# Performance work log

Measured on AMD Instinct MI355X. Metric: run time of the kernel, lower is better.

## Reference

```python
import jax, jax.numpy as jnp
import numpy as np

EPS = 1e-9
WINDOW = 5
TEMP = 1.0


def _ln(x, g, b):
    m = jnp.mean(x, -1, keepdims=True)
    v = jnp.mean((x - m) ** 2, -1, keepdims=True)
    return (x - m) * jax.lax.rsqrt(v + 1e-5) * g + b


def setup_inputs() -> dict:
    key = jax.random.key(0)
    ks = jax.random.split(key, 20)
    N, S, D, H, W = 32, 512, 256, 1024, WINDOW
    sd = 0.02
    inp = {
        'sequence': jax.random.normal(ks[0], (N, S, D), jnp.float32),
        'input_mask': jnp.ones((N, S, 1), jnp.float32),
        'START': jax.random.normal(ks[1], (D,), jnp.float32),
        'END': jax.random.normal(ks[2], (D,), jnp.float32),
        'yes_t': jax.random.normal(ks[3], (1, 1, D), jnp.float32),
        'no_t': jax.random.normal(ks[4], (1, 1, D), jnp.float32),
        'convW': jax.random.normal(ks[5], (W * D, D), jnp.float32) * sd,
        'convb': jnp.zeros((D,), jnp.float32),
        'scW': jax.random.normal(ks[6], (D, 1), jnp.float32) * sd,
        'scb': jnp.zeros((1,), jnp.float32),
        'itW': jax.random.normal(ks[7], (D, D), jnp.float32) * sd,
        'itb': jnp.zeros((D,), jnp.float32),
        'w1W': jax.random.normal(ks[8], (2 * D, H), jnp.float32) * sd,
        'w1b': jnp.zeros((H,), jnp.float32),
        'w2W': jax.random.normal(ks[9], (H, 4 * D), jnp.float32) * sd,
        'w2b': jnp.zeros((4 * D,), jnp.float32),
        'lng': jnp.ones((D,), jnp.float32),
        'lnb': jnp.zeros((D,), jnp.float32),
        'n_steps': 6,
    }
    return inp


def _forward(sequence, input_mask, START, END, yes_t, no_t, convW, convb, scW, scb,
             itW, itb, w1W, w1b, w2W, w2b, lng, lnb, n_steps):
    N, S, D = sequence.shape
    dt = sequence.dtype
    # ---- augment_sequence: add soft START / END tokens ----
    seq = jnp.concatenate([jnp.broadcast_to(START.reshape(1, 1, D), (N, 1, D)), sequence], 1)
    mask = jnp.concatenate([jnp.ones((N, 1, 1), dt), input_mask], 1)            # (N,S+1,1)
    mask_no_end = jnp.concatenate([mask, jnp.zeros((N, 1, 1), dt)], 1)          # (N,S+2,1)
    mask_yes_end = jnp.concatenate([jnp.ones((N, 1, 1), dt), mask], 1)
    END_mask = mask_yes_end - mask_no_end
    seq = jnp.concatenate([seq, jnp.zeros((N, 1, D), dt)], 1)                   # (N,S+2,D)
    seq = END_mask * END.reshape(1, 1, D) + (1 - END_mask) * seq
    mask = mask_yes_end
    mask_no_start = jnp.concatenate([jnp.zeros((N, 1, 1), dt), mask[:, 1:]], 1)
    S2 = S + 2
    last_token_mask = jnp.concatenate([END_mask[:, 1:], jnp.zeros((N, 1, 1), dt)], 1)
    selp = mask_no_start * mask_no_end * (1.0 - last_token_mask)                # START_END_LAST_PAD_mask

    active = jnp.ones((N, S2, 1), dt) * mask
    ltp = jnp.zeros((N, S2, 1), dt)
    seq = _ln(seq @ itW + itb, lng, lnb) * mask                                 # initial_transform

    def neighbor_probs(active, mask):
        am = jnp.swapaxes(mask, 1, 2)                                           # (N,1,S2)
        ap = jnp.swapaxes(active, 1, 2)
        am2 = jnp.stack([am[:, :, ::-1], am], 1)                                # (N,2,1,S2)
        ap2 = jnp.stack([ap[:, :, ::-1], ap], 1)
        mat = jnp.broadcast_to(ap2, (N, 2, S2, S2)) * am2                       # (N,2,S2,S2)
        right_exist = jnp.triu(mat, 1)
        log_not = jnp.triu(jnp.log(1.0 - right_exist + EPS), 1)
        not_yet = jnp.exp(jnp.cumsum(log_not, -1))
        not_yet = jnp.concatenate([jnp.ones((N, 2, S2, 1), dt), not_yet[..., :-1]], -1)
        rp = right_exist * not_yet * am2
        left = rp[:, 0][:, ::-1, ::-1]                                          # flip dims (1,2)
        right = rp[:, 1]
        return left, right

    for _ in range(n_steps):
        lnp, rnp = neighbor_probs(active, mask)
        tf = ltp * yes_t + (1 - ltp) * no_t
        base = seq + tf
        lk, rk = base, base
        lefts, rights = [], []
        for _k in range(WINDOW // 2):                                           # k-hop soft neighbors
            lk = lnp @ lk
            lefts = [lk] + lefts
            rk = rnp @ rk
            rights = rights + [rk]
        ws = jnp.stack(lefts + [base] + rights, -2)                             # (N,S2,W,D)
        flat = ws.reshape(N, S2, WINDOW * D)
        tsc = (jax.nn.gelu(flat @ convW + convb) @ scW + scb)[..., 0:1] / TEMP
        mx = jnp.maximum(jnp.max(tsc), 0.0)                                     # no-op score is 0
        et = jnp.exp(tsc - mx) * selp
        en = jnp.exp(-mx)
        tp = et / (et + en + EPS)                                               # transition prob
        # ---- composer (gated cell) on (left child, self) ----
        left_child = lnp @ seq
        cc = jnp.concatenate([left_child, seq], -1)
        inter = jax.nn.gelu(cc @ w1W + w1b)
        contents = (inter @ w2W + w2b).reshape(N, S2, 4, D)
        gates = jax.nn.sigmoid(contents[:, :, :3])
        parent = contents[:, :, 3]
        comp = _ln(gates[:, :, 0] * left_child + gates[:, :, 1] * seq + gates[:, :, 2] * parent, lng, lnb)
        seq = (tp * comp + (1 - tp) * seq) * mask
        # left child of a transitioning node becomes inactive
        deact = jnp.einsum('bij,bi->bj', lnp, tp[..., 0])[..., None]
        active = jnp.clip(active * (1.0 - deact), 0.0, 1.0) * mask
        ltp = tp
    return seq


def reference(sequence, input_mask, START, END, yes_t, no_t, convW, convb, scW, scb,
              itW, itb, w1W, w1b, w2W, w2b, lng, lnb, n_steps):
    return _forward(sequence, input_mask, START, END, yes_t, no_t, convW, convb, scW, scb,
                    itW, itb, w1W, w1b, w2W, w2b, lng, lnb, int(n_steps))
```

## Files before the change

kernel.cpp:

```cpp
#include <hip/hip_runtime.h>
#include <math.h>

#define NB 32
#define SS 512
#define S2 514
#define DD 256
#define HH 1024
#define MS (NB*S2)
#define MP 16512
#define EPSF 1e-9f
#define NSTEPS 6
#define NCH 9

typedef unsigned short ushort_t;
typedef __attribute__((ext_vector_type(8))) short short8;
typedef __attribute__((ext_vector_type(4))) float f32x4;

__device__ __forceinline__ float gelu_f(float x){
  float t = tanhf(0.7978845608028654f*(x + 0.044715f*x*x*x));
  return 0.5f*x*(1.f+t);
}
__device__ __forceinline__ float sigmoid_f(float x){ return 1.f/(1.f+expf(-x)); }
__device__ __forceinline__ ushort_t f2bf(float f){
  unsigned u = __float_as_uint(f);
  u += 0x7fffu + ((u>>16)&1u);
  return (ushort_t)(u>>16);
}
__device__ __forceinline__ float bf2f(ushort_t b){
  return __uint_as_float(((unsigned)b)<<16);
}
__device__ __forceinline__ void gload_lds16(const void* g, void* l){
  __builtin_amdgcn_global_load_lds((const __attribute__((address_space(1))) void*)g,
                                   (__attribute__((address_space(3))) void*)l, 16, 0, 0);
}

__global__ __launch_bounds__(256) void k_wt(const float* __restrict__ W, ushort_t* __restrict__ WT,
                                            int K, int N){
  __shared__ float t[64][65];
  int k0 = blockIdx.x*64, n0 = blockIdx.y*64;
  int tx = threadIdx.x & 63, ty = threadIdx.x >> 6;
#pragma unroll
  for (int i=ty;i<64;i+=4) t[i][tx] = W[(size_t)(k0+i)*N + n0 + tx];
  __syncthreads();
#pragma unroll
  for (int i=ty;i<64;i+=4) WT[(size_t)(n0+i)*K + k0 + tx] = f2bf(t[tx][i]);
}

__global__ void k_build_seq0(const float* __restrict__ seq_in, const float* __restrict__ START,
                             const float* __restrict__ END, ushort_t* __restrict__ out){
  int m = blockIdx.x; int d = threadIdx.x;
  int s = m % S2; int b = m / S2;
  float v;
  if (s == 0)        v = START[d];
  else if (s <= SS)  v = seq_in[((size_t)(b*SS + (s-1)))*DD + d];
  else               v = END[d];
  out[(size_t)m*DD + d] = f2bf(v);
}

__global__ void k_init_state(float* __restrict__ ltp, float* __restrict__ act){
  int i = blockIdx.x*256 + threadIdx.x;
  if (i < MS){ ltp[i]=0.f; act[i]=1.f; }
}

template<int ACT, int OUTBF, int SCORE>
__global__ __launch_bounds__(256) void k_mgemm(const ushort_t* __restrict__ A,
    const ushort_t* __restrict__ BT, const float* __restrict__ bias,
    float* __restrict__ Cf, ushort_t* __restrict__ Cb,
    const float* __restrict__ scW, float* __restrict__ tsc,
    int M, int N, int K)
{
  __shared__ __align__(16) ushort_t Asm[2][128*32];
  __shared__ __align__(16) ushort_t Bsm[2][128*32];
  const int tid = threadIdx.x;
  const int lane = tid & 63, wid = tid >> 6;

  const int nwg = gridDim.x, f = blockIdx.x;
  const int q = nwg >> 3, r = nwg & 7;
  const int x = f & 7, jj = f >> 3;
  const int logical = (x < r ? x*(q+1) : r*(q+1) + (x-r)*q) + jj;
  const int NX = N >> 7;
  const int bx = logical % NX, by = logical / NX;
  const int m0 = by * 128, n0 = bx * 128;
  const int wr = (wid>>1)*64, wc = (wid&1)*64;

  f32x4 acc[4][4];
#pragma unroll
  for (int i=0;i<4;i++)
#pragma unroll
    for (int j=0;j<4;j++) acc[i][j] = (f32x4){0.f,0.f,0.f,0.f};

  const int srow4 = lane >> 2;
  const int scol = ((((lane&3) - (lane>>3)) & 3) << 3);
  const int rrow = lane & 15, rhi = lane >> 4;

  const int nt = K >> 5;
  int cur = 0;

#pragma unroll
  for (int tt=0; tt<2; ++tt){
    int c = wid + 4*tt;
    gload_lds16(A  + (size_t)(m0 + c*16 + srow4)*K + scol, &Asm[0][c*512]);
    gload_lds16(BT + (size_t)(n0 + c*16 + srow4)*K + scol, &Bsm[0][c*512]);
  }
  asm volatile("s_waitcnt vmcnt(0)\n\ts_barrier" ::: "memory");

  for (int t=0; t<nt; ++t){
    if (t+1 < nt){
      const int k1 = (t+1) << 5;
#pragma unroll
      for (int tt=0; tt<2; ++tt){
        int c = wid + 4*tt;
        gload_lds16(A  + (size_t)(m0 + c*16 + srow4)*K + k1 + scol, &Asm[cur^1][c*512]);
        gload_lds16(BT + (size_t)(n0 + c*16 + srow4)*K + k1 + scol, &Bsm[cur^1][c*512]);
      }
    }
    short8 a[4], b[4];
#pragma unroll
    for (int i=0;i<4;i++){
      int ra = wr + i*16 + rrow;
      int sa = ((rhi + (ra>>1)) & 3) << 3;
      a[i] = *reinterpret_cast<const short8*>(&Asm[cur][ra*32 + sa]);
      int rb = wc + i*16 + rrow;
      int sb = ((rhi + (rb>>1)) & 3) << 3;
      b[i] = *reinterpret_cast<const short8*>(&Bsm[cur][rb*32 + sb]);
    }
    __builtin_amdgcn_s_setprio(1);
#pragma unroll
    for (int i=0;i<4;i++)
#pragma unroll
      for (int j=0;j<4;j++)
        acc[i][j] = __builtin_amdgcn_mfma_f32_16x16x32_bf16(a[i], b[j], acc[i][j], 0,0,0);
    __builtin_amdgcn_s_setprio(0);
    if (t+1 < nt){
      asm volatile("s_waitcnt vmcnt(0)\n\ts_barrier" ::: "memory");
      cur ^= 1;
    }
  }

  if (SCORE){
#pragma unroll
    for (int i=0;i<4;i++){
#pragma unroll
      for (int rreg=0;rreg<4;rreg++){
        float rs = 0.f;
#pragma unroll
        for (int j=0;j<4;j++){
          int gn = n0 + wc + j*16 + (lane&15);
          float v = gelu_f(acc[i][j][rreg] + bias[gn]);
          rs += v * scW[gn];
        }
        rs += __shfl_xor(rs,1); rs += __shfl_xor(rs,2);
        rs += __shfl_xor(rs,4); rs += __shfl_xor(rs,8);
        if ((lane&15)==0){
          int gm = m0 + wr + i*16 + (lane>>4)*4 + rreg;
          atomicAdd(&tsc[gm], rs);
        }
      }
    }
  } else {
#pragma unroll
    for (int i=0;i<4;i++){
#pragma unroll
      for (int rreg=0;rreg<4;rreg++){
        size_t gm = m0 + wr + i*16 + (lane>>4)*4 + rreg;
#pragma unroll
        for (int j=0;j<4;j++){
          int gn = n0 + wc + j*16 + (lane&15);
          float v = acc[i][j][rreg] + bias[gn];
          if (ACT==1) v = gelu_f(v);
          if (OUTBF) Cb[gm*N + gn] = f2bf(v);
          else       Cf[gm*N + gn] = v;
        }
      }
    }
  }
}

__global__ __launch_bounds__(256) void k_ln(const float* __restrict__ x, const float* __restrict__ g,
                                            const float* __restrict__ bta, float* __restrict__ out,
                                            ushort_t* __restrict__ cc){
  __shared__ float red[8];
  int m = blockIdx.x, d = threadIdx.x;
  float v = x[(size_t)m*DD + d];
  float s1 = v, s2 = v*v;
  for (int off=32; off; off>>=1){ s1 += __shfl_down(s1,off); s2 += __shfl_down(s2,off); }
  int wid = d >> 6;
  if ((d&63)==0){ red[wid*2]=s1; red[wid*2+1]=s2; }
  __syncthreads();
  float sum = red[0]+red[2]+red[4]+red[6];
  float sq  = red[1]+red[3]+red[5]+red[7];
  float mean = sum * (1.f/DD);
  float var  = sq  * (1.f/DD) - mean*mean;
  float inv  = rsqrtf(fmaxf(var,0.f) + 1e-5f);
  float o = (v-mean)*inv*g[d] + bta[d];
  out[(size_t)m*DD + d] = o;
  cc[(size_t)m*(2*DD) + DD + d] = f2bf(o);
}

template<int PASS>
__global__ __launch_bounds__(64) void k_scanchunk(
    const ushort_t* __restrict__ ccp, const float* __restrict__ ltpp, const float* __restrict__ actp,
    const float* __restrict__ yes_t, const float* __restrict__ no_t,
    ushort_t* __restrict__ ws5, ushort_t* __restrict__ ccw,
    float* __restrict__ carry, float* __restrict__ scal)
{
  __shared__ ushort_t s_sv[66][64];
  __shared__ float s_lt[66], s_ac[66];
  const int b = blockIdx.x, dg = blockIdx.y & 3, ck = blockIdx.y >> 2, dir = blockIdx.z, t = threadIdx.x;
  int st, ln;
  if (dir==0){ st = ck*64; ln = (S2 - st < 64) ? (S2 - st) : 64; }
  else { int hi = (S2-1) - ck*64; st = (hi-63 < 0) ? 0 : hi-63; ln = hi - st + 1; }
  const int lo = st - 1;
  const size_t mb = (size_t)b*S2;
  for (int r=0; r<ln+2; ++r){
    int gr = lo + r; gr = gr < 0 ? 0 : (gr > S2-1 ? S2-1 : gr);
    s_sv[r][t] = ccp[(mb+gr)*(2*DD) + DD + (dg<<6) + t];
  }
  for (int r=t; r<ln+2; r+=64){
    int gr = lo + r; gr = gr < 0 ? 0 : (gr > S2-1 ? S2-1 : gr);
    s_lt[r] = ltpp[mb+gr]; s_ac[r] = actp[mb+gr];
  }
  __syncthreads();
  const int d = (dg<<6)+t;
  const float yv = yes_t[d], nv = no_t[d];
  float ci1=0.f, ci2=0.f, cic=0.f;
  const size_t cbase = (((size_t)b*2+dir)*NCH + ck)*3*DD;
  if (PASS==1){
    ci1 = carry[cbase+d]; ci2 = carry[cbase+DD+d];
    if (dir==0) cic = carry[cbase+2*DD+d];
  }
  float A=1.f, Bs=0.f, z1=0.f, z2=0.f, zc=0.f;
  const int pr = (dir==0) ? 0 : (ln+1);
  float svp = bf2f(s_sv[pr][t]); float ltpv = s_lt[pr];
  float pb = svp + ltpv*yv + (1.f-ltpv)*nv, ps = svp, pa = s_ac[pr];
  for (int i=0;i<ln;i++){
    const int r = (dir==0) ? (i+1) : (ln-i);
    const int s = (dir==0) ? (st+i) : (st+ln-1-i);
    float sv = bf2f(s_sv[r][t]); float lt = s_lt[r]; float av = s_ac[r];
    float bse = sv + lt*yv + (1.f-lt)*nv;
    bool upd = (dir==0) ? (s>0) : (s<S2-1);
    if (upd){
      float c = pa, fc = 1.f-c+EPSF;
      z2 = c*z1 + fc*z2;
      z1 = c*pb + fc*z1;
      zc = c*ps + fc*zc;
      Bs = c*A + fc*Bs; A = fc*A;
    }
    if (PASS==1){
      size_t m = mb + s; size_t w5 = m*(5*DD);
      float Z1 = z1 + A*ci1, Z2 = z2 + Bs*ci1 + A*ci2;
      if (dir==0){
        float Zc = zc + A*cic;
        ws5[w5 + d]        = f2bf(Z2);
        ws5[w5 + DD + d]   = f2bf(Z1);
        ws5[w5 + 2*DD + d] = f2bf(bse);
        ccw[m*(2*DD) + d]  = f2bf(Zc);
      } else {
        ws5[w5 + 3*DD + d] = f2bf(Z1);
        ws5[w5 + 4*DD + d] = f2bf(Z2);
      }
    }
    pb=bse; ps=sv; pa=av;
  }
  if (PASS==0){
    carry[cbase+d] = z1; carry[cbase+DD+d] = z2;
    if (dir==0) carry[cbase+2*DD+d] = zc;
    if (dg==0 && t==0){ size_t sb = (((size_t)b*2+dir)*NCH+ck)*2; scal[sb]=A; scal[sb+1]=Bs; }
  }
}

__global__ __launch_bounds__(64) void k_scancomb(const float* __restrict__ cl, float* __restrict__ cin,
    const float* __restrict__ scal, float* __restrict__ tscp, const float* __restrict__ scb,
    unsigned* __restrict__ mxp)
{
  const int b = blockIdx.x, dg = blockIdx.y, dir = blockIdx.z, t = threadIdx.x;
  const int d = (dg<<6)+t;
  if (dir==0 && dg==0){
    float sbv = scb[0];
    for (int i=t;i<S2;i+=64) tscp[(size_t)b*S2+i]=sbv;
    if (b==0 && t==0) *mxp = 0u;
  }
  float s1=0.f,s2=0.f,sc=0.f;
  for (int k=0;k<NCH;k++){
    size_t cbase = (((size_t)b*2+dir)*NCH+k)*3*DD;
    cin[cbase+d]=s1; cin[cbase+DD+d]=s2; if(dir==0) cin[cbase+2*DD+d]=sc;
    size_t sb = (((size_t)b*2+dir)*NCH+k)*2;
    float A = scal[sb], Bs = scal[sb+1];
    float l1 = cl[cbase+d], l2 = cl[cbase+DD+d];
    float ns1 = l1 + A*s1;
    float ns2 = l2 + Bs*s1 + A*s2;
    if (dir==0){ float lcv = cl[cbase+2*DD+d]; sc = lcv + A*sc; }
    s1=ns1; s2=ns2;
  }
}

__global__ __launch_bounds__(256) void k_maxred(const float* __restrict__ tsc, unsigned* __restrict__ mx){
  __shared__ float red[4];
  int t0 = blockIdx.x*256 + threadIdx.x;
  float v = 0.f;
  for (int i=t0; i<MS; i+=256*32) v = fmaxf(v, tsc[i]);
  for (int off=32; off; off>>=1) v = fmaxf(v, __shfl_down(v,off));
  if ((threadIdx.x&63)==0) red[threadIdx.x>>6]=v;
  __syncthreads();
  if (threadIdx.x==0){
    float r = fmaxf(fmaxf(red[0],red[1]),fmaxf(red[2],red[3]));
    atomicMax(mx, __float_as_uint(r));
  }
}

__global__ __launch_bounds__(256) void k_epi(const ushort_t* __restrict__ contents,
     const float* __restrict__ tsc, const unsigned* __restrict__ mx,
     const float* __restrict__ g, const float* __restrict__ bta,
     float* __restrict__ seq, ushort_t* __restrict__ cc, float* __restrict__ ltp){
  __shared__ float red[8];
  int m = blockIdx.x, d = threadIdx.x;
  int s = m % S2;
  float M = __uint_as_float(*mx);
  float sel = (s >= 1 && s <= SS-1) ? 1.f : 0.f;
  float et = expf(tsc[m]-M)*sel;
  float tpv = et/(et+expf(-M)+EPSF);
  if (d==0) ltp[m] = tpv;

  size_t b4 = (size_t)m*HH;
  float lcv = bf2f(cc[(size_t)m*(2*DD) + d]);
  float sv  = seq[(size_t)m*DD+d];
  float g0 = sigmoid_f(bf2f(contents[b4 + d]));
  float g1 = sigmoid_f(bf2f(contents[b4 + DD + d]));
  float g2 = sigmoid_f(bf2f(contents[b4 + 2*DD + d]));
  float pv = bf2f(contents[b4 + 3*DD + d]);
  float xv = g0*lcv + g1*sv + g2*pv;
  float s1=xv, s2=xv*xv;
  for (int off=32; off; off>>=1){ s1 += __shfl_down(s1,off); s2 += __shfl_down(s2,off); }
  int wid = d>>6;
  if ((d&63)==0){ red[wid*2]=s1; red[wid*2+1]=s2; }
  __syncthreads();
  float sum=red[0]+red[2]+red[4]+red[6];
  float sq =red[1]+red[3]+red[5]+red[7];
  float mean = sum*(1.f/DD);
  float var  = sq *(1.f/DD)-mean*mean;
  float inv = rsqrtf(fmaxf(var,0.f)+1e-5f);
  float comp = (xv-mean)*inv*g[d] + bta[d];
  float o = tpv*comp + (1.f-tpv)*sv;
  seq[(size_t)m*DD+d] = o;
  cc[(size_t)m*(2*DD) + DD + d] = f2bf(o);
}

__global__ __launch_bounds__(64) void k_actup(const float* __restrict__ tp, float* __restrict__ act){
  __shared__ float s_a[S2], s_t[S2], s_o[S2];
  int b = blockIdx.x, t = threadIdx.x;
  for (int s=t;s<S2;s+=64){ s_a[s]=act[(size_t)b*S2+s]; s_t[s]=tp[(size_t)b*S2+s]; }
  __syncthreads();
  int hi = (S2-1) - 9*t;
  int lo = hi - 8; if (lo < 0) lo = 0;
  float A=1.f, Bv=0.f;
  if (hi >= 0){
    for (int s=hi; s>=lo; --s){
      float fc = 1.f - s_a[s] + EPSF;
      Bv = s_t[s] + fc*Bv; A = fc*A;
    }
  }
  float Ai=A, Bi=Bv;
  for (int off=1; off<64; off<<=1){
    float Ao = __shfl_up(Ai, off), Bo = __shfl_up(Bi, off);
    if (t >= off){ Bi = Bi + Ai*Bo; Ai = Ai*Ao; }
  }
  float uin = __shfl_up(Bi, 1); if (t==0) uin = 0.f;
  if (hi >= 0){
    float u = uin;
    for (int s=hi; s>=lo; --s){
      float a = s_a[s];
      float na = a*(1.f - a*u);
      s_o[s] = fminf(fmaxf(na,0.f),1.f);
      u = s_t[s] + (1.f - a + EPSF)*u;
    }
  }
  __syncthreads();
  for (int s=t;s<S2;s+=64) act[(size_t)b*S2+s]=s_o[s];
}

extern "C" void kernel_launch(void* const* d_in, const int* in_sizes, int n_in,
                              void* d_out, int out_size, void* d_ws, size_t ws_size,
                              hipStream_t stream){
  const float* seq_in = (const float*)d_in[0];
  const float* START = (const float*)d_in[2];
  const float* END   = (const float*)d_in[3];
  const float* yes_t = (const float*)d_in[4];
  const float* no_t  = (const float*)d_in[5];
  const float* convW = (const float*)d_in[6];
  const float* convb = (const float*)d_in[7];
  const float* scW   = (const float*)d_in[8];
  const float* scb   = (const float*)d_in[9];
  const float* itW   = (const float*)d_in[10];
  const float* itb   = (const float*)d_in[11];
  const float* w1W   = (const float*)d_in[12];
  const float* w1b   = (const float*)d_in[13];
  const float* w2W   = (const float*)d_in[14];
  const float* w2b   = (const float*)d_in[15];
  const float* lng   = (const float*)d_in[16];
  const float* lnb   = (const float*)d_in[17];

  char* p = (char*)d_ws;
  float*    seq  = (float*)p;    p += (size_t)MP*DD*4;
  ushort_t* cc   = (ushort_t*)p; p += (size_t)MP*(2*DD)*2;
  ushort_t* ws5      = (ushort_t*)p;
  ushort_t* contents = (ushort_t*)p;
  float*    preLN    = (float*)p; p += (size_t)MP*2560;
  ushort_t* inter = (ushort_t*)p;
  ushort_t* seq0  = (ushort_t*)p; p += (size_t)MP*2048;
  ushort_t* itWT   = (ushort_t*)p; p += (size_t)256*256*2;
  ushort_t* convWT = (ushort_t*)p; p += (size_t)256*1280*2;
  ushort_t* w1WT   = (ushort_t*)p; p += (size_t)1024*512*2;
  ushort_t* w2WT   = (ushort_t*)p; p += (size_t)1024*1024*2;
  float* ltp = (float*)p; p += (size_t)MS*4;
  float* act = (float*)p; p += (size_t)MS*4;
  float* tsc = (float*)p; p += (size_t)MP*4;
  unsigned* mx = (unsigned*)p; p += 256;
  float* carryL = (float*)p; p += (size_t)NB*2*NCH*3*DD*4;
  float* carryI = (float*)p; p += (size_t)NB*2*NCH*3*DD*4;
  float* scal   = (float*)p; p += (size_t)NB*2*NCH*2*4;

  dim3 b256(256), b64(64);

  { dim3 g(256/64, 256/64);   k_wt<<<g, b256, 0, stream>>>(itW,  itWT,  256, 256); }
  { dim3 g(1280/64, 256/64);  k_wt<<<g, b256, 0, stream>>>(convW,convWT,1280,256); }
  { dim3 g(512/64, 1024/64);  k_wt<<<g, b256, 0, stream>>>(w1W,  w1WT,  512, 1024); }
  { dim3 g(1024/64, 1024/64); k_wt<<<g, b256, 0, stream>>>(w2W,  w2WT,  1024,1024); }

  k_build_seq0<<<MS, 256, 0, stream>>>(seq_in, START, END, seq0);
  { int nwg = (256/128)*(MP/128);
    k_mgemm<0,0,0><<<nwg, b256, 0, stream>>>(seq0, itWT, itb, preLN, nullptr, nullptr, nullptr, MP, 256, 256); }
  k_ln<<<MS, 256, 0, stream>>>(preLN, lng, lnb, seq, cc);
  k_init_state<<<(MS+255)/256, 256, 0, stream>>>(ltp, act);

  for (int step=0; step<NSTEPS; ++step){
    { dim3 g(NB, 4*NCH, 2);
      k_scanchunk<0><<<g, b64, 0, stream>>>(cc, ltp, act, yes_t, no_t, ws5, cc, carryL, scal); }
    { dim3 g(NB, 4, 2);
      k_scancomb<<<g, b64, 0, stream>>>(carryL, carryI, scal, tsc, scb, mx); }
    { dim3 g(NB, 4*NCH, 2);
      k_scanchunk<1><<<g, b64, 0, stream>>>(cc, ltp, act, yes_t, no_t, ws5, cc, carryI, scal); }
    { int nwg = (256/128)*(MP/128);
      k_mgemm<0,0,1><<<nwg, b256, 0, stream>>>(ws5, convWT, convb, nullptr, nullptr, scW, tsc, MP, 256, 5*DD); }
    k_maxred<<<32, b256, 0, stream>>>(tsc, mx);
    { int nwg = (HH/128)*(MP/128);
      k_mgemm<1,1,0><<<nwg, b256, 0, stream>>>(cc, w1WT, w1b, nullptr, inter, nullptr, nullptr, MP, HH, 2*DD); }
    { int nwg = (HH/128)*(MP/128);
      k_mgemm<0,1,0><<<nwg, b256, 0, stream>>>(inter, w2WT, w2b, nullptr, contents, nullptr, nullptr, MP, HH, HH); }
    k_epi<<<MS, 256, 0, stream>>>(contents, tsc, mx, lng, lnb, seq, cc, ltp);
    k_actup<<<NB, b64, 0, stream>>>(ltp, act);
  }
  hipMemcpyAsync(d_out, seq, (size_t)out_size*sizeof(float), hipMemcpyDeviceToDevice, stream);
}
```

Measured before the change: 1.376 ms.

## Fuse scan combine and max-reduction into neighbours; use 128x64 tiles for N=256 GEMMs

Removes the separate scan-combine kernel by having each pass-1 chunk recompute its carry-in from the preceding chunk summaries, and moves tsc/mx initialisation into pass-0. The global max-reduction over scores is folded into the first 32 blocks of the w1 GEMM, and the N=256 GEMMs switch to 128x64 tiles to launch more workgroups. This cuts two launches per step and improves occupancy for narrow GEMMs, at the cost of redundant carry recomputation and extra work in some GEMM blocks.

```diff
diff --git a/kernel.cpp b/kernel.cpp
--- a/kernel.cpp
+++ b/kernel.cpp
@@ -62,30 +62,47 @@
   if (i < MS){ ltp[i]=0.f; act[i]=1.f; }
 }
 
-template<int ACT, int OUTBF, int SCORE>
+template<int ACT, int OUTBF, int SCORE, int NTILE, int DOMAX>
 __global__ __launch_bounds__(256) void k_mgemm(const ushort_t* __restrict__ A,
     const ushort_t* __restrict__ BT, const float* __restrict__ bias,
     float* __restrict__ Cf, ushort_t* __restrict__ Cb,
-    const float* __restrict__ scW, float* __restrict__ tsc,
+    const float* __restrict__ scW, float* __restrict__ tsc, unsigned* __restrict__ mxp,
     int M, int N, int K)
 {
   __shared__ __align__(16) ushort_t Asm[2][128*32];
-  __shared__ __align__(16) ushort_t Bsm[2][128*32];
+  __shared__ __align__(16) ushort_t Bsm[2][NTILE*32];
   const int tid = threadIdx.x;
   const int lane = tid & 63, wid = tid >> 6;
+
+  if (DOMAX){
+    if (blockIdx.x < 32){
+      __shared__ float redm[4];
+      float v = 0.f;
+      for (int i = blockIdx.x*256 + tid; i < MS; i += 8192) v = fmaxf(v, tsc[i]);
+      for (int off=32; off; off>>=1) v = fmaxf(v, __shfl_down(v,off));
+      if ((tid&63)==0) redm[tid>>6]=v;
+      __syncthreads();
+      if (tid==0){
+        float r = fmaxf(fmaxf(redm[0],redm[1]),fmaxf(redm[2],redm[3]));
+        atomicMax(mxp, __float_as_uint(r));
+      }
+    }
+  }
 
   const int nwg = gridDim.x, f = blockIdx.x;
   const int q = nwg >> 3, r = nwg & 7;
   const int x = f & 7, jj = f >> 3;
   const int logical = (x < r ? x*(q+1) : r*(q+1) + (x-r)*q) + jj;
-  const int NX = N >> 7;
+  const int NX = N / NTILE;
   const int bx = logical % NX, by = logical / NX;
-  const int m0 = by * 128, n0 = bx * 128;
-  const int wr = (wid>>1)*64, wc = (wid&1)*64;
+  const int m0 = by * 128, n0 = bx * NTILE;
+  const int MI = (NTILE==128) ? 4 : 2;
+  const int wr = (NTILE==128) ? (wid>>1)*64 : wid*32;
+  const int wc = (NTILE==128) ? (wid&1)*64  : 0;
 
   f32x4 acc[4][4];
 #pragma unroll
-  for (int i=0;i<4;i++)
+  for (int i=0;i<MI;i++)
 #pragma unroll
     for (int j=0;j<4;j++) acc[i][j] = (f32x4){0.f,0.f,0.f,0.f};
 
@@ -94,39 +111,41 @@
   const int rrow = lane & 15, rhi = lane >> 4;
 
   const int nt = K >> 5;
+
+#define STAGE_T(tt_, bi_)                                                              \
+  {                                                                                    \
+    const int k0_ = (tt_) << 5;                                                        \
+    _Pragma("unroll")                                                                  \
+    for (int cc_=0; cc_<2; ++cc_){                                                     \
+      int c_ = wid + 4*cc_;                                                            \
+      gload_lds16(A + (size_t)(m0 + c_*16 + srow4)*K + k0_ + scol, &Asm[bi_][c_*512]); \
+      if (NTILE==128 || cc_==0)                                                        \
+        gload_lds16(BT + (size_t)(n0 + c_*16 + srow4)*K + k0_ + scol, &Bsm[bi_][c_*512]); \
+    }                                                                                  \
+  }
+
+  STAGE_T(0, 0);
+  asm volatile("s_waitcnt vmcnt(0)\n\ts_barrier" ::: "memory");
+
   int cur = 0;
-
-#pragma unroll
-  for (int tt=0; tt<2; ++tt){
-    int c = wid + 4*tt;
-    gload_lds16(A  + (size_t)(m0 + c*16 + srow4)*K + scol, &Asm[0][c*512]);
-    gload_lds16(BT + (size_t)(n0 + c*16 + srow4)*K + scol, &Bsm[0][c*512]);
-  }
-  asm volatile("s_waitcnt vmcnt(0)\n\ts_barrier" ::: "memory");
-
   for (int t=0; t<nt; ++t){
-    if (t+1 < nt){
-      const int k1 = (t+1) << 5;
-#pragma unroll
-      for (int tt=0; tt<2; ++tt){
-        int c = wid + 4*tt;
-        gload_lds16(A  + (size_t)(m0 + c*16 + srow4)*K + k1 + scol, &Asm[cur^1][c*512]);
-        gload_lds16(BT + (size_t)(n0 + c*16 + srow4)*K + k1 + scol, &Bsm[cur^1][c*512]);
-      }
-    }
+    if (t+1 < nt) STAGE_T(t+1, cur^1);
     short8 a[4], b[4];
 #pragma unroll
-    for (int i=0;i<4;i++){
+    for (int i=0;i<MI;i++){
       int ra = wr + i*16 + rrow;
       int sa = ((rhi + (ra>>1)) & 3) << 3;
       a[i] = *reinterpret_cast<const short8*>(&Asm[cur][ra*32 + sa]);
-      int rb = wc + i*16 + rrow;
+    }
+#pragma unroll
+    for (int j=0;j<4;j++){
+      int rb = wc + j*16 + rrow;
       int sb = ((rhi + (rb>>1)) & 3) << 3;
-      b[i] = *reinterpret_cast<const short8*>(&Bsm[cur][rb*32 + sb]);
+      b[j] = *reinterpret_cast<const short8*>(&Bsm[cur][rb*32 + sb]);
     }
     __builtin_amdgcn_s_setprio(1);
 #pragma unroll
-    for (int i=0;i<4;i++)
+    for (int i=0;i<MI;i++)
 #pragma unroll
       for (int j=0;j<4;j++)
         acc[i][j] = __builtin_amdgcn_mfma_f32_16x16x32_bf16(a[i], b[j], acc[i][j], 0,0,0);
@@ -136,10 +155,11 @@
       cur ^= 1;
     }
   }
+#undef STAGE_T
 
   if (SCORE){
 #pragma unroll
-    for (int i=0;i<4;i++){
+    for (int i=0;i<MI;i++){
 #pragma unroll
       for (int rreg=0;rreg<4;rreg++){
         float rs = 0.f;
@@ -159,7 +179,7 @@
     }
   } else {
 #pragma unroll
-    for (int i=0;i<4;i++){
+    for (int i=0;i<MI;i++){
 #pragma unroll
       for (int rreg=0;rreg<4;rreg++){
         size_t gm = m0 + wr + i*16 + (lane>>4)*4 + rreg;
@@ -202,16 +222,24 @@
     const ushort_t* __restrict__ ccp, const float* __restrict__ ltpp, const float* __restrict__ actp,
     const float* __restrict__ yes_t, const float* __restrict__ no_t,
     ushort_t* __restrict__ ws5, ushort_t* __restrict__ ccw,
-    float* __restrict__ carry, float* __restrict__ scal)
+    float* __restrict__ carry, float* __restrict__ scal,
+    float* __restrict__ tscp, const float* __restrict__ scb, unsigned* __restrict__ mxp)
 {
   __shared__ ushort_t s_sv[66][64];
   __shared__ float s_lt[66], s_ac[66];
   const int b = blockIdx.x, dg = blockIdx.y & 3, ck = blockIdx.y >> 2, dir = blockIdx.z, t = threadIdx.x;
+  const size_t mb = (size_t)b*S2;
+
+  if (PASS==0 && dir==0 && dg==0 && ck==0){
+    float sbv = scb[0];
+    for (int i=t;i<S2;i+=64) tscp[mb+i]=sbv;
+    if (b==0 && t==0) *mxp = 0u;
+  }
+
   int st, ln;
   if (dir==0){ st = ck*64; ln = (S2 - st < 64) ? (S2 - st) : 64; }
   else { int hi = (S2-1) - ck*64; st = (hi-63 < 0) ? 0 : hi-63; ln = hi - st + 1; }
   const int lo = st - 1;
-  const size_t mb = (size_t)b*S2;
   for (int r=0; r<ln+2; ++r){
     int gr = lo + r; gr = gr < 0 ? 0 : (gr > S2-1 ? S2-1 : gr);
     s_sv[r][t] = ccp[(mb+gr)*(2*DD) + DD + (dg<<6) + t];
@@ -226,8 +254,18 @@
   float ci1=0.f, ci2=0.f, cic=0.f;
   const size_t cbase = (((size_t)b*2+dir)*NCH + ck)*3*DD;
   if (PASS==1){
-    ci1 = carry[cbase+d]; ci2 = carry[cbase+DD+d];
-    if (dir==0) cic = carry[cbase+2*DD+d];
+    float s1=0.f, s2=0.f, sc=0.f;
+    for (int k=0;k<ck;k++){
+      size_t cb2 = (((size_t)b*2+dir)*NCH + k)*3*DD;
+      size_t sb = (((size_t)b*2+dir)*NCH + k)*2;
+      float Ak = scal[sb], Bk = scal[sb+1];
+      float l1 = carry[cb2+d], l2 = carry[cb2+DD+d];
+      float ns1 = l1 + Ak*s1;
+      float ns2 = l2 + Bk*s1 + Ak*s2;
+      if (dir==0){ sc = carry[cb2+2*DD+d] + Ak*sc; }
+      s1=ns1; s2=ns2;
+    }
+    ci1=s1; ci2=s2; cic=sc;
   }
   float A=1.f, Bs=0.f, z1=0.f, z2=0.f, zc=0.f;
   const int pr = (dir==0) ? 0 : (ln+1);
@@ -266,45 +304,6 @@
     carry[cbase+d] = z1; carry[cbase+DD+d] = z2;
     if (dir==0) carry[cbase+2*DD+d] = zc;
     if (dg==0 && t==0){ size_t sb = (((size_t)b*2+dir)*NCH+ck)*2; scal[sb]=A; scal[sb+1]=Bs; }
-  }
-}
-
-__global__ __launch_bounds__(64) void k_scancomb(const float* __restrict__ cl, float* __restrict__ cin,
-    const float* __restrict__ scal, float* __restrict__ tscp, const float* __restrict__ scb,
-    unsigned* __restrict__ mxp)
-{
-  const int b = blockIdx.x, dg = blockIdx.y, dir = blockIdx.z, t = threadIdx.x;
-  const int d = (dg<<6)+t;
-  if (dir==0 && dg==0){
-    float sbv = scb[0];
-    for (int i=t;i<S2;i+=64) tscp[(size_t)b*S2+i]=sbv;
-    if (b==0 && t==0) *mxp = 0u;
-  }
-  float s1=0.f,s2=0.f,sc=0.f;
-  for (int k=0;k<NCH;k++){
-    size_t cbase = (((size_t)b*2+dir)*NCH+k)*3*DD;
-    cin[cbase+d]=s1; cin[cbase+DD+d]=s2; if(dir==0) cin[cbase+2*DD+d]=sc;
-    size_t sb = (((size_t)b*2+dir)*NCH+k)*2;
-    float A = scal[sb], Bs = scal[sb+1];
-    float l1 = cl[cbase+d], l2 = cl[cbase+DD+d];
-    float ns1 = l1 + A*s1;
-    float ns2 = l2 + Bs*s1 + A*s2;
-    if (dir==0){ float lcv = cl[cbase+2*DD+d]; sc = lcv + A*sc; }
-    s1=ns1; s2=ns2;
-  }
-}
-
-__global__ __launch_bounds__(256) void k_maxred(const float* __restrict__ tsc, unsigned* __restrict__ mx){
-  __shared__ float red[4];
-  int t0 = blockIdx.x*256 + threadIdx.x;
-  float v = 0.f;
-  for (int i=t0; i<MS; i+=256*32) v = fmaxf(v, tsc[i]);
-  for (int off=32; off; off>>=1) v = fmaxf(v, __shfl_down(v,off));
-  if ((threadIdx.x&63)==0) red[threadIdx.x>>6]=v;
-  __syncthreads();
-  if (threadIdx.x==0){
-    float r = fmaxf(fmaxf(red[0],red[1]),fmaxf(red[2],red[3]));
-    atomicMax(mx, __float_as_uint(r));
   }
 }
 
@@ -416,7 +415,6 @@
   float* tsc = (float*)p; p += (size_t)MP*4;
   unsigned* mx = (unsigned*)p; p += 256;
   float* carryL = (float*)p; p += (size_t)NB*2*NCH*3*DD*4;
-  float* carryI = (float*)p; p += (size_t)NB*2*NCH*3*DD*4;
   float* scal   = (float*)p; p += (size_t)NB*2*NCH*2*4;
 
   dim3 b256(256), b64(64);
@@ -427,25 +425,22 @@
   { dim3 g(1024/64, 1024/64); k_wt<<<g, b256, 0, stream>>>(w2W,  w2WT,  1024,1024); }
 
   k_build_seq0<<<MS, 256, 0, stream>>>(seq_in, START, END, seq0);
-  { int nwg = (256/128)*(MP/128);
-    k_mgemm<0,0,0><<<nwg, b256, 0, stream>>>(seq0, itWT, itb, preLN, nullptr, nullptr, nullptr, MP, 256, 256); }
+  { int nwg = (256/64)*(MP/128);
+    k_mgemm<0,0,0,64,0><<<nwg, b256, 0, stream>>>(seq0, itWT, itb, preLN, nullptr, nullptr, nullptr, nullptr, MP, 256, 256); }
   k_ln<<<MS, 256, 0, stream>>>(preLN, lng, lnb, seq, cc);
   k_init_state<<<(MS+255)/256, 256, 0, stream>>>(ltp, act);
 
   for (int step=0; step<NSTEPS; ++step){
     { dim3 g(NB, 4*NCH, 2);
-      k_scanchunk<0><<<g, b64, 0, stream>>>(cc, ltp, act, yes_t, no_t, ws5, cc, carryL, scal); }
-    { dim3 g(NB, 4, 2);
-      k_scancomb<<<g, b64, 0, stream>>>(carryL, carryI, scal, tsc, scb, mx); }
+      k_scanchunk<0><<<g, b64, 0, stream>>>(cc, ltp, act, yes_t, no_t, ws5, cc, carryL, scal, tsc, scb, mx); }
     { dim3 g(NB, 4*NCH, 2);
-      k_scanchunk<1><<<g, b64, 0, stream>>>(cc, ltp, act, yes_t, no_t, ws5, cc, carryI, scal); }
-    { int nwg = (256/128)*(MP/128);
-      k_mgemm<0,0,1><<<nwg, b256, 0, stream>>>(ws5, convWT, convb, nullptr, nullptr, scW, tsc, MP, 256, 5*DD); }
-    k_maxred<<<32, b256, 0, stream>>>(tsc, mx);
+      k_scanchunk<1><<<g, b64, 0, stream>>>(cc, ltp, act, yes_t, no_t, ws5, cc, carryL, scal, tsc, scb, mx); }
+    { int nwg = (256/64)*(MP/128);
+      k_mgemm<0,0,1,64,0><<<nwg, b256, 0, stream>>>(ws5, convWT, convb, nullptr, nullptr, scW, tsc, nullptr, MP, 256, 5*DD); }
     { int nwg = (HH/128)*(MP/128);
-      k_mgemm<1,1,0><<<nwg, b256, 0, stream>>>(cc, w1WT, w1b, nullptr, inter, nullptr, nullptr, MP, HH, 2*DD); }
+      k_mgemm<1,1,0,128,1><<<nwg, b256, 0, stream>>>(cc, w1WT, w1b, nullptr, inter, nullptr, tsc, mx, MP, HH, 2*DD); }
     { int nwg = (HH/128)*(MP/128);
-      k_mgemm<0,1,0><<<nwg, b256, 0, stream>>>(inter, w2WT, w2b, nullptr, contents, nullptr, nullptr, MP, HH, HH); }
+      k_mgemm<0,1,0,128,0><<<nwg, b256, 0, stream>>>(inter, w2WT, w2b, nullptr, contents, nullptr, nullptr, nullptr, MP, HH, HH); }
     k_epi<<<MS, 256, 0, stream>>>(contents, tsc, mx, lng, lnb, seq, cc, ltp);
     k_actup<<<NB, b64, 0, stream>>>(ltp, act);
   }
```

Result: faster. 1.293 ms (-6.0%).
